# Performance work log

Hardware: AMD Instinct MI355X
Metric: run time of the kernel (lower is better)

## Reference

```python
import jax, jax.numpy as jnp
import numpy as np

K_NN = 2       # module's k (kNN count)
ALPHA = 1.1    # threshold = mean + alpha * std


def setup_inputs() -> dict:
    key = jax.random.key(0)
    x = jax.random.normal(key, (4, 8192, 3), dtype=jnp.float32)  # [B, K, 3]
    return {"x": x}


def reference(x):
    # Statistical outlier removal (SOR). Torch version runs the distance /
    # mask computation on a detached copy -> stop_gradient here.
    pc = jax.lax.stop_gradient(x)                      # [B, K, 3]
    xx = jnp.sum(pc * pc, axis=-1)                     # [B, K]
    # squared pairwise distances: ||a||^2 - 2 a.b + ||b||^2  -> [B, K, K]
    dist = xx[:, :, None] - 2.0 * jnp.einsum('bkd,bjd->bkj', pc, pc) + xx[:, None, :]
    # kNN distances: take k+1 smallest (incl. self at distance ~0), drop self
    neg_val, _ = jax.lax.top_k(-dist, K_NN + 1)        # [B, K, k+1]
    value = jnp.mean(-neg_val[..., 1:], axis=-1)       # [B, K] mean kNN dist
    mean = jnp.mean(value, axis=-1)                    # [B]
    std = jnp.std(value, axis=-1, ddof=1)              # [B] unbiased (torch.std)
    threshold = mean + ALPHA * std                     # [B]
    mask = value <= threshold[:, None]                 # [B, K] keep-mask
    # Torch returns a ragged list x[i][mask[i]]; for a jit-able fixed-shape
    # reference we return the masked (zero-padded) points plus the mask.
    masked_pc = x * mask[..., None].astype(x.dtype)    # [B, K, 3]
    return masked_pc, mask
```

## Files before the change

kernel.cpp:

```cpp
#include <hip/hip_runtime.h>
#include <math.h>


constexpr int B = 4;
constexpr int K = 8192;
constexpr int QPB = 256;
constexpr int QPT = 4;
constexpr int QBLK = QPB * QPT;

#define BIG 3.0e38f

#define MINSERT(d, e0, e1, e2)                                  \
  do {                                                          \
    const float n0_ = fminf((e0), (d));                         \
    const float n1_ = __builtin_amdgcn_fmed3f((d), (e0), (e1)); \
    const float n2_ = __builtin_amdgcn_fmed3f((d), (e1), (e2)); \
    (e0) = n0_; (e1) = n1_; (e2) = n2_;                         \
  } while (0)

#define PQ_STEP(P, Q)                                                   \
  do {                                                                  \
    const float dot_ = (qx[Q] * (P).x + qy[Q] * (P).y) + qz[Q] * (P).z; \
    const float d_ = (qn[Q] - 2.0f * dot_) + (P).w;                     \
    MINSERT(d_, e0[Q], e1[Q], e2[Q]);                                   \
  } while (0)

template <int CHUNK>
__global__ __launch_bounds__(QPB, 4) void knn_part_kernel(
    const float* __restrict__ x, float* __restrict__ part) {
  constexpr int NCH = K / CHUNK;
  const int bid   = blockIdx.x;
  const int chunk = bid % NCH;
  const int rest  = bid / NCH;
  const int kc    = rest % (K / QBLK);
  const int b     = rest / (K / QBLK);
  const int tid   = threadIdx.x;

  const float* xb = x + (size_t)b * K * 3;

  float qx[QPT], qy[QPT], qz[QPT], qn[QPT];
#pragma unroll
  for (int q = 0; q < QPT; ++q) {
    const int k = kc * QBLK + q * QPB + tid;
    qx[q] = xb[(size_t)k * 3 + 0];
    qy[q] = xb[(size_t)k * 3 + 1];
    qz[q] = xb[(size_t)k * 3 + 2];
    qn[q] = (qx[q] * qx[q] + qy[q] * qy[q]) + qz[q] * qz[q];
  }

  __shared__ float4 s[CHUNK];
  const int jbase = chunk * CHUNK;
  for (int i = tid; i < CHUNK; i += QPB) {
    const float px = xb[(size_t)(jbase + i) * 3 + 0];
    const float py = xb[(size_t)(jbase + i) * 3 + 1];
    const float pz = xb[(size_t)(jbase + i) * 3 + 2];
    s[i] = make_float4(px, py, pz, (px * px + py * py) + pz * pz);
  }
  __syncthreads();

  float e0[QPT], e1[QPT], e2[QPT];
#pragma unroll
  for (int q = 0; q < QPT; ++q) { e0[q] = BIG; e1[q] = BIG; e2[q] = BIG; }

  for (int j = 0; j < CHUNK; j += 8) {
    float4 pts[8];
#pragma unroll
    for (int u = 0; u < 8; ++u) pts[u] = s[j + u];
#pragma unroll
    for (int u = 0; u < 8; ++u) {
#pragma unroll
      for (int q = 0; q < QPT; ++q) {
        PQ_STEP(pts[u], q);
      }
    }
  }

#pragma unroll
  for (int q = 0; q < QPT; ++q) {
    const int k = kc * QBLK + q * QPB + tid;
    float* pp = part + ((size_t)(b * K + k) * NCH + chunk) * 3;
    pp[0] = e0[q];
    pp[1] = e1[q];
    pp[2] = e2[q];
  }
}

template <int NCH>
__global__ __launch_bounds__(256) void sor_value_kernel(
    const float* __restrict__ part, float* __restrict__ value,
    double* __restrict__ bsum) {
  const int blk = blockIdx.x;
  const int b   = blk >> 5;
  const int tid = threadIdx.x;
  const int k   = (blk & 31) * 256 + tid;

  const float* pp = part + (size_t)(b * K + k) * NCH * 3;
  float d0 = BIG, d1 = BIG, d2 = BIG;
#pragma unroll
  for (int t = 0; t < NCH * 3; ++t) {
    const float d = pp[t];
    MINSERT(d, d0, d1, d2);
  }
  const float v = 0.5f * (d1 + d2);
  value[b * K + k] = v;

  double s = (double)v, s2 = (double)v * (double)v;
  for (int off = 32; off > 0; off >>= 1) {
    s  += __shfl_down(s, off, 64);
    s2 += __shfl_down(s2, off, 64);
  }
  __shared__ double rs[4], rs2[4];
  const int wave = tid >> 6;
  if ((tid & 63) == 0) { rs[wave] = s; rs2[wave] = s2; }
  __syncthreads();
  if (tid == 0) {
    double S = 0.0, S2 = 0.0;
    for (int w = 0; w < 4; ++w) { S += rs[w]; S2 += rs2[w]; }
    bsum[blk * 2 + 0] = S;
    bsum[blk * 2 + 1] = S2;
  }
}

__global__ __launch_bounds__(64) void sor_thresh_kernel(
    const double* __restrict__ bsum, float* __restrict__ thr) {
  const int b = threadIdx.x;
  if (b < B) {
    double S = 0.0, S2 = 0.0;
    for (int w = 0; w < 32; ++w) {
      S  += bsum[(b * 32 + w) * 2 + 0];
      S2 += bsum[(b * 32 + w) * 2 + 1];
    }
    const double mean = S / (double)K;
    const double var  = (S2 - S * S / (double)K) / (double)(K - 1);
    thr[b] = (float)(mean + 1.1 * sqrt(var));
  }
}

__global__ __launch_bounds__(256) void sor_mask_kernel(
    const float* __restrict__ x, const float* __restrict__ value,
    const float* __restrict__ thr, float* __restrict__ out) {
  const int g = blockIdx.x * 256 + threadIdx.x;
  const int b = g / K;
  const float m = (value[g] <= thr[b]) ? 1.0f : 0.0f;
  out[(size_t)B * K * 3 + g] = m;
  const size_t base = (size_t)g * 3;
  out[base + 0] = x[base + 0] * m;
  out[base + 1] = x[base + 1] * m;
  out[base + 2] = x[base + 2] * m;
}

template <int NCH>
static void run(const float* x, float* out, char* ws, hipStream_t stream) {
  float* part = (float*)ws;
  size_t off = (size_t)B * K * NCH * 3 * sizeof(float);
  float* value = (float*)(ws + off);
  off += (size_t)B * K * sizeof(float);
  off = (off + 7) & ~(size_t)7;
  double* bsum = (double*)(ws + off);
  off += (size_t)B * 32 * 2 * sizeof(double);
  float* thr = (float*)(ws + off);

  knn_part_kernel<K / NCH><<<B * (K / QBLK) * NCH, QPB, 0, stream>>>(x, part);
  sor_value_kernel<NCH><<<B * 32, 256, 0, stream>>>(part, value, bsum);
  sor_thresh_kernel<<<1, 64, 0, stream>>>(bsum, thr);
  sor_mask_kernel<<<B * K / 256, 256, 0, stream>>>(x, value, thr, out);
}

extern "C" void kernel_launch(void* const* d_in, const int* in_sizes, int n_in,
                              void* d_out, int out_size, void* d_ws, size_t ws_size,
                              hipStream_t stream) {
  const float* x = (const float*)d_in[0];
  float* out = (float*)d_out;
  char* ws = (char*)d_ws;

  const size_t extra = (size_t)B * K * sizeof(float) + 4096;
  if (ws_size >= (size_t)B * K * 32 * 3 * sizeof(float) + extra) {
    run<32>(x, out, ws, stream);
  } else if (ws_size >= (size_t)B * K * 16 * 3 * sizeof(float) + extra) {
    run<16>(x, out, ws, stream);
  } else if (ws_size >= (size_t)B * K * 8 * 3 * sizeof(float) + extra) {
    run<8>(x, out, ws, stream);
  } else {
    run<2>(x, out, ws, stream);
  }
}
```

Measured before the change: 75.17 us.

## Stream candidate points via scalar loads from prepacked float4 buffer instead of LDS

```diff
diff --git a/kernel.cpp b/kernel.cpp
--- a/kernel.cpp
+++ b/kernel.cpp
@@ -9,6 +9,8 @@
 constexpr int QBLK = QPB * QPT;
 
 #define BIG 3.0e38f
+
+using f32x16 = __attribute__((ext_vector_type(16))) float;
 
 #define MINSERT(d, e0, e1, e2)                                  \
   do {                                                          \
@@ -18,16 +20,25 @@
     (e0) = n0_; (e1) = n1_; (e2) = n2_;                         \
   } while (0)
 
-#define PQ_STEP(P, Q)                                                   \
-  do {                                                                  \
-    const float dot_ = (qx[Q] * (P).x + qy[Q] * (P).y) + qz[Q] * (P).z; \
-    const float d_ = (qn[Q] - 2.0f * dot_) + (P).w;                     \
-    MINSERT(d_, e0[Q], e1[Q], e2[Q]);                                   \
+#define PQ1(PX, PY, PZ, PW, Q)                                        \
+  do {                                                                \
+    const float dot_ = (qx[Q] * (PX) + qy[Q] * (PY)) + qz[Q] * (PZ);  \
+    const float d_ = (qn[Q] - 2.0f * dot_) + (PW);                    \
+    MINSERT(d_, e0[Q], e1[Q], e2[Q]);                                 \
   } while (0)
+
+__global__ __launch_bounds__(256) void pack_kernel(
+    const float* __restrict__ x, float4* __restrict__ pack) {
+  const int g = blockIdx.x * 256 + threadIdx.x;
+  const float px = x[(size_t)g * 3 + 0];
+  const float py = x[(size_t)g * 3 + 1];
+  const float pz = x[(size_t)g * 3 + 2];
+  pack[g] = make_float4(px, py, pz, (px * px + py * py) + pz * pz);
+}
 
 template <int CHUNK>
 __global__ __launch_bounds__(QPB, 4) void knn_part_kernel(
-    const float* __restrict__ x, float* __restrict__ part) {
+    const float4* __restrict__ pack, float* __restrict__ part) {
   constexpr int NCH = K / CHUNK;
   const int bid   = blockIdx.x;
   const int chunk = bid % NCH;
@@ -36,52 +47,48 @@
   const int b     = rest / (K / QBLK);
   const int tid   = threadIdx.x;
 
-  const float* xb = x + (size_t)b * K * 3;
+  const float4* pb = pack + (size_t)b * K;
 
   float qx[QPT], qy[QPT], qz[QPT], qn[QPT];
+#pragma unroll
+  for (int q = 0; q < QPT; ++q) {
+    const float4 f = pb[kc * QBLK + q * QPB + tid];
+    qx[q] = f.x; qy[q] = f.y; qz[q] = f.z; qn[q] = f.w;
+  }
+
+  float e0[QPT], e1[QPT], e2[QPT];
+#pragma unroll
+  for (int q = 0; q < QPT; ++q) { e0[q] = BIG; e1[q] = BIG; e2[q] = BIG; }
+
+  const float4* pp = pb + chunk * CHUNK;
+  for (int j = 0; j < CHUNK; j += 8, pp += 8) {
+    f32x16 c0, c1;
+    asm volatile("s_load_dwordx16 %0, %1, 0x0" : "=s"(c0) : "s"(pp));
+    asm volatile("s_load_dwordx16 %0, %1, 0x0" : "=s"(c1) : "s"(pp + 4));
+    asm volatile("s_waitcnt lgkmcnt(0)" : "+s"(c0), "+s"(c1));
+#pragma unroll
+    for (int u = 0; u < 4; ++u) {
+#pragma unroll
+      for (int q = 0; q < QPT; ++q) {
+        PQ1(c0[4 * u + 0], c0[4 * u + 1], c0[4 * u + 2], c0[4 * u + 3], q);
+      }
+    }
+#pragma unroll
+    for (int u = 0; u < 4; ++u) {
+#pragma unroll
+      for (int q = 0; q < QPT; ++q) {
+        PQ1(c1[4 * u + 0], c1[4 * u + 1], c1[4 * u + 2], c1[4 * u + 3], q);
+      }
+    }
+  }
+
 #pragma unroll
   for (int q = 0; q < QPT; ++q) {
     const int k = kc * QBLK + q * QPB + tid;
-    qx[q] = xb[(size_t)k * 3 + 0];
-    qy[q] = xb[(size_t)k * 3 + 1];
-    qz[q] = xb[(size_t)k * 3 + 2];
-    qn[q] = (qx[q] * qx[q] + qy[q] * qy[q]) + qz[q] * qz[q];
-  }
-
-  __shared__ float4 s[CHUNK];
-  const int jbase = chunk * CHUNK;
-  for (int i = tid; i < CHUNK; i += QPB) {
-    const float px = xb[(size_t)(jbase + i) * 3 + 0];
-    const float py = xb[(size_t)(jbase + i) * 3 + 1];
-    const float pz = xb[(size_t)(jbase + i) * 3 + 2];
-    s[i] = make_float4(px, py, pz, (px * px + py * py) + pz * pz);
-  }
-  __syncthreads();
-
-  float e0[QPT], e1[QPT], e2[QPT];
-#pragma unroll
-  for (int q = 0; q < QPT; ++q) { e0[q] = BIG; e1[q] = BIG; e2[q] = BIG; }
-
-  for (int j = 0; j < CHUNK; j += 8) {
-    float4 pts[8];
-#pragma unroll
-    for (int u = 0; u < 8; ++u) pts[u] = s[j + u];
-#pragma unroll
-    for (int u = 0; u < 8; ++u) {
-#pragma unroll
-      for (int q = 0; q < QPT; ++q) {
-        PQ_STEP(pts[u], q);
-      }
-    }
-  }
-
-#pragma unroll
-  for (int q = 0; q < QPT; ++q) {
-    const int k = kc * QBLK + q * QPB + tid;
-    float* pp = part + ((size_t)(b * K + k) * NCH + chunk) * 3;
-    pp[0] = e0[q];
-    pp[1] = e1[q];
-    pp[2] = e2[q];
+    float* dst = part + ((size_t)chunk * (B * K) + (size_t)b * K + k) * 3;
+    dst[0] = e0[q];
+    dst[1] = e1[q];
+    dst[2] = e2[q];
   }
 }
 
@@ -94,12 +101,17 @@
   const int tid = threadIdx.x;
   const int k   = (blk & 31) * 256 + tid;
 
-  const float* pp = part + (size_t)(b * K + k) * NCH * 3;
+  const float* pp = part + (size_t)(b * K + k) * 3;
   float d0 = BIG, d1 = BIG, d2 = BIG;
-#pragma unroll
-  for (int t = 0; t < NCH * 3; ++t) {
-    const float d = pp[t];
-    MINSERT(d, d0, d1, d2);
+#pragma unroll 4
+  for (int ch = 0; ch < NCH; ++ch) {
+    const float a0 = pp[0];
+    const float a1 = pp[1];
+    const float a2 = pp[2];
+    MINSERT(a0, d0, d1, d2);
+    MINSERT(a1, d0, d1, d2);
+    MINSERT(a2, d0, d1, d2);
+    pp += (size_t)B * K * 3;
   }
   const float v = 0.5f * (d1 + d2);
   value[b * K + k] = v;
@@ -151,8 +163,10 @@
 
 template <int NCH>
 static void run(const float* x, float* out, char* ws, hipStream_t stream) {
-  float* part = (float*)ws;
-  size_t off = (size_t)B * K * NCH * 3 * sizeof(float);
+  float4* pack = (float4*)ws;
+  size_t off = (size_t)B * K * sizeof(float4);
+  float* part = (float*)(ws + off);
+  off += (size_t)B * K * NCH * 3 * sizeof(float);
   float* value = (float*)(ws + off);
   off += (size_t)B * K * sizeof(float);
   off = (off + 7) & ~(size_t)7;
@@ -160,7 +174,8 @@
   off += (size_t)B * 32 * 2 * sizeof(double);
   float* thr = (float*)(ws + off);
 
-  knn_part_kernel<K / NCH><<<B * (K / QBLK) * NCH, QPB, 0, stream>>>(x, part);
+  pack_kernel<<<B * K / 256, 256, 0, stream>>>(x, pack);
+  knn_part_kernel<K / NCH><<<B * (K / QBLK) * NCH, QPB, 0, stream>>>(pack, part);
   sor_value_kernel<NCH><<<B * 32, 256, 0, stream>>>(part, value, bsum);
   sor_thresh_kernel<<<1, 64, 0, stream>>>(bsum, thr);
   sor_mask_kernel<<<B * K / 256, 256, 0, stream>>>(x, value, thr, out);
@@ -173,12 +188,13 @@
   float* out = (float*)d_out;
   char* ws = (char*)d_ws;
 
-  const size_t extra = (size_t)B * K * sizeof(float) + 4096;
-  if (ws_size >= (size_t)B * K * 32 * 3 * sizeof(float) + extra) {
+  const size_t fixed = (size_t)B * K * sizeof(float4) +
+                       (size_t)B * K * sizeof(float) + 4096;
+  if (ws_size >= (size_t)B * K * 32 * 3 * sizeof(float) + fixed) {
     run<32>(x, out, ws, stream);
-  } else if (ws_size >= (size_t)B * K * 16 * 3 * sizeof(float) + extra) {
+  } else if (ws_size >= (size_t)B * K * 16 * 3 * sizeof(float) + fixed) {
     run<16>(x, out, ws, stream);
-  } else if (ws_size >= (size_t)B * K * 8 * 3 * sizeof(float) + extra) {
+  } else if (ws_size >= (size_t)B * K * 8 * 3 * sizeof(float) + fixed) {
     run<8>(x, out, ws, stream);
   } else {
     run<2>(x, out, ws, stream);
```

Measured after the change: 76.02 us. About the same (+1.1%).
